# Kernel optimization log

Measured on AMD Instinct MI355X. Metric: run time of the kernel, lower is better.

## Reference

```python
import jax, jax.numpy as jnp
import numpy as np

DIM, HEADS, WH, WW = 96, 3, 7, 7
N = WH * WW            # 49 tokens per window
NW = 64                # windows per image (56x56 / 7x7)
B = 64                 # images
BNW = B * NW           # 4096


def _relative_position_index(Wh, Ww):
    coords = np.stack(np.meshgrid(np.arange(Wh), np.arange(Ww), indexing='ij'))
    coords = coords.reshape(2, -1)                       # (2, Wh*Ww)
    rel = coords[:, :, None] - coords[:, None, :]        # (2, N, N)
    rel = rel.transpose(1, 2, 0).copy()                  # (N, N, 2)
    rel[..., 0] += Wh - 1
    rel[..., 1] += Ww - 1
    rel[..., 0] *= 2 * Ww - 1
    return jnp.asarray(rel.sum(-1), dtype=jnp.int32)     # (N, N)


def setup_inputs() -> dict:
    key = jax.random.key(0)
    ks = jax.random.split(key, 8)
    x = jax.random.normal(ks[0], (BNW, N, DIM), dtype=jnp.float32)
    # shifted-window style additive mask: 0 where allowed, -100 where blocked
    mask = jnp.where(jax.random.uniform(ks[1], (NW, N, N)) < 0.9, 0.0, -100.0).astype(jnp.float32)
    qkv_w = jax.random.normal(ks[2], (3 * DIM, DIM), dtype=jnp.float32) * 0.02
    qkv_b = jnp.zeros((3 * DIM,), dtype=jnp.float32)
    proj_w = jax.random.normal(ks[3], (DIM, DIM), dtype=jnp.float32) * 0.02
    proj_b = jnp.zeros((DIM,), dtype=jnp.float32)
    rpb_table = jax.random.normal(ks[4], ((2 * WH - 1) * (2 * WW - 1), HEADS), dtype=jnp.float32) * 0.02
    rel_index = _relative_position_index(WH, WW)
    return {"x": x, "mask": mask, "qkv_w": qkv_w, "qkv_b": qkv_b,
            "proj_w": proj_w, "proj_b": proj_b, "rpb_table": rpb_table,
            "rel_index": rel_index}


def reference(x, mask, qkv_w, qkv_b, proj_w, proj_b, rpb_table, rel_index):
    BnW, n, C = x.shape
    H = rpb_table.shape[-1]
    hd = C // H
    scale = hd ** -0.5
    qkv = (x @ qkv_w.T + qkv_b).reshape(BnW, n, 3, H, hd)
    qkv = jnp.transpose(qkv, (2, 0, 3, 1, 4))            # (3, BnW, H, N, hd)
    q, k, v = qkv[0] * scale, qkv[1], qkv[2]
    attn = jnp.einsum('bhnd,bhmd->bhnm', q, k)           # (BnW, H, N, N)
    bias = rpb_table[rel_index.reshape(-1)].reshape(n, n, H)
    attn = attn + jnp.transpose(bias, (2, 0, 1))[None]
    nW = mask.shape[0]
    attn = attn.reshape(BnW // nW, nW, H, n, n) + mask[None, :, None]
    attn = attn.reshape(BnW, H, n, n)
    # 'neg' softmax: sign(x) * softmax(|x|)
    attn = jnp.sign(attn) * jax.nn.softmax(jnp.abs(attn), axis=-1)
    out = jnp.einsum('bhnm,bhmd->bnhd', attn, v).reshape(BnW, n, C)
    return out @ proj_w.T + proj_b
```

## Files before the change

kernel.cpp:

```cpp
#include <hip/hip_runtime.h>
#include <math.h>

#define DIM    96
#define HEADS  3
#define NTOK   49
#define NWIN   64
#define SCALE  0.17677669529663687f
#define MW     2

#define PROJWB_OFFB 55296
#define TAB_OFFB    73728
#define FUSED_TAB_ELEMS (NWIN * HEADS * NTOK * NTOK)
#define BIAS_TAB_ELEMS  (HEADS * NTOK * NTOK)
#define WS_MODE2_NEED (TAB_OFFB + FUSED_TAB_ELEMS * 4)
#define WS_MODE1_NEED (TAB_OFFB + BIAS_TAB_ELEMS * 4)

#define WSTRIDE 12288
#define K_OFF   0
#define VT_OFF  6144
#define LDS_SHORTS (MW * WSTRIDE)

typedef float  f32x4   __attribute__((ext_vector_type(4)));
typedef __bf16 bf16x8  __attribute__((ext_vector_type(8)));
typedef short  short8  __attribute__((ext_vector_type(8)));
typedef __bf16 bf16x4  __attribute__((ext_vector_type(4)));
typedef short  short4v __attribute__((ext_vector_type(4)));

union U8 { short8  s; bf16x8 b; };
union U4 { short4v s; bf16x4 b; };

__device__ __forceinline__ int swz(int s) { return s ^ ((s >> 3) & 56); }

__device__ __forceinline__ unsigned short f2bf(float f) {
    __bf16 h = (__bf16)f;
    union { __bf16 h; unsigned short u; } v; v.h = h; return v.u;
}

__device__ __forceinline__ void ldcvt_g(const float* __restrict__ p, U8& u) {
    float4 f0 = *(const float4*)p;
    float4 f1 = *(const float4*)(p + 4);
    u.b[0] = (__bf16)f0.x; u.b[1] = (__bf16)f0.y; u.b[2] = (__bf16)f0.z; u.b[3] = (__bf16)f0.w;
    u.b[4] = (__bf16)f1.x; u.b[5] = (__bf16)f1.y; u.b[6] = (__bf16)f1.z; u.b[7] = (__bf16)f1.w;
}

__global__ __launch_bounds__(256)
void prep(const float* __restrict__ rpb, const int* __restrict__ rel,
          const float* __restrict__ mask,
          const float* __restrict__ qkv_w, const float* __restrict__ proj_w,
          unsigned short* __restrict__ qkv_wb, unsigned short* __restrict__ proj_wb,
          float* __restrict__ tab, int mode)
{
    int t = blockIdx.x * 256 + threadIdx.x;
    if (mode >= 1) {
        if (t < 3 * DIM * DIM) qkv_wb[t] = f2bf(qkv_w[t]);
        if (t < DIM * DIM)     proj_wb[t] = f2bf(proj_w[t]);
    }
    if (mode == 2) {
        if (t < FUSED_TAB_ELEMS) {
            int win = t / (HEADS * NTOK * NTOK);
            int rem = t - win * (HEADS * NTOK * NTOK);
            int h   = rem / (NTOK * NTOK);
            int ij  = rem - h * (NTOK * NTOK);
            int k = ij / NTOK, q = ij - k * NTOK;
            tab[t] = rpb[rel[q * NTOK + k] * HEADS + h] + mask[win * (NTOK * NTOK) + q * NTOK + k];
        }
    } else if (t < BIAS_TAB_ELEMS) {
        int h = t / (NTOK * NTOK), ij = t - h * (NTOK * NTOK);
        int k = ij / NTOK, q = ij - k * NTOK;
        tab[t] = rpb[rel[q * NTOK + k] * HEADS + h];
    }
}

template<int MODE>
__device__ __forceinline__ void ldw(const unsigned short* __restrict__ wb,
                                    const float* __restrict__ wf, int idx, U8& u) {
    if constexpr (MODE >= 1) u.s = *(const short8*)(wb + idx);
    else                     ldcvt_g(wf + idx, u);
}
template<int MODE>
__device__ __forceinline__ void ldw4(const unsigned short* __restrict__ wb,
                                     const float* __restrict__ wf, int idx, U4& u) {
    if constexpr (MODE >= 1) u.s = *(const short4v*)(wb + idx);
    else {
        float4 f = *(const float4*)(wf + idx);
        u.b[0] = (__bf16)f.x; u.b[1] = (__bf16)f.y; u.b[2] = (__bf16)f.z; u.b[3] = (__bf16)f.w;
    }
}

template<int MODE>
__global__ __launch_bounds__(256, 3)
void winattn(const float* __restrict__ x,
             const float* __restrict__ mask,
             const float* __restrict__ qkv_w,
             const float* __restrict__ qkv_b,
             const float* __restrict__ proj_w,
             const float* __restrict__ proj_b,
             const unsigned short* __restrict__ qkv_wb,
             const unsigned short* __restrict__ proj_wb,
             const float* __restrict__ tab,
             float* __restrict__ out, int nwin_tot)
{
    __shared__ __align__(16) unsigned short sbuf[LDS_SHORTS];

    const int tid  = threadIdx.x;
    const int lane = tid & 63;
    const int wave = __builtin_amdgcn_readfirstlane(tid >> 6);
    const int l15  = lane & 15;
    const int quad = lane >> 4;
    const int tokg = 16 * wave + l15;
    const int qcl  = (tokg < NTOK) ? tokg : (NTOK - 1);

    int bw[MW];
    const float* fmh[MW][3];
    const float* mww[MW];
    #pragma unroll
    for (int w = 0; w < MW; ++w) {
        int b = blockIdx.x * MW + w;
        bw[w] = (b < nwin_tot) ? b : (nwin_tot - 1);
        const int win = bw[w] & (NWIN - 1);
        #pragma unroll
        for (int h = 0; h < 3; ++h)
            fmh[w][h] = (MODE == 2) ? (tab + (size_t)(win * HEADS + h) * (NTOK * NTOK))
                                    : (tab + h * (NTOK * NTOK));
        mww[w] = mask + (size_t)win * (NTOK * NTOK);
    }

    U8 af[MW][3];
    #pragma unroll
    for (int w = 0; w < MW; ++w) {
        const float* xw = x + (size_t)bw[w] * (NTOK * DIM);
        #pragma unroll
        for (int s = 0; s < 3; ++s) {
            if (tokg < NTOK) ldcvt_g(xw + tokg * DIM + 32 * s + quad * 8, af[w][s]);
            else {
                #pragma unroll
                for (int j = 0; j < 8; ++j) af[w][s].b[j] = (__bf16)0.0f;
            }
        }
    }

    U4 qB[MW][3][2];
    U8 wpf[2][3];
    f32x4 qbp[2];
    #pragma unroll
    for (int s = 0; s < 3; ++s) {
        ldw<MODE>(qkv_wb, qkv_w, (l15) * DIM + 32 * s + quad * 8, wpf[0][s]);
        ldw<MODE>(qkv_wb, qkv_w, (16 + l15) * DIM + 32 * s + quad * 8, wpf[1][s]);
    }
    qbp[0] = *(const f32x4*)(qkv_b + quad * 4);
    qbp[1] = *(const f32x4*)(qkv_b + 16 + quad * 4);

    #pragma unroll
    for (int t = 0; t < 18; ++t) {
        f32x4 acc[MW];
        #pragma unroll
        for (int w = 0; w < MW; ++w) {
            f32x4 z = {0.f, 0.f, 0.f, 0.f};
            #pragma unroll
            for (int s = 0; s < 3; ++s)
                z = __builtin_amdgcn_mfma_f32_16x16x32_bf16(wpf[t & 1][s].b, af[w][s].b, z, 0, 0, 0);
            acc[w] = z;
        }
        f32x4 qb = qbp[t & 1];
        if (t + 2 < 18) {
            #pragma unroll
            for (int s = 0; s < 3; ++s)
                ldw<MODE>(qkv_wb, qkv_w, (16 * (t + 2) + l15) * DIM + 32 * s + quad * 8, wpf[t & 1][s]);
            qbp[t & 1] = *(const f32x4*)(qkv_b + 16 * (t + 2) + quad * 4);
        }
        if (t < 6) {
            const int h = t >> 1, half = t & 1;
            #pragma unroll
            for (int w = 0; w < MW; ++w)
                #pragma unroll
                for (int r = 0; r < 4; ++r)
                    qB[w][h][half].b[r] = (__bf16)((acc[w][r] + qb[r]) * SCALE);
        } else if (t < 12) {
            const int tt = t - 6, h = tt >> 1, dc = tt & 1;
            #pragma unroll
            for (int w = 0; w < MW; ++w) {
                U4 pk;
                #pragma unroll
                for (int r = 0; r < 4; ++r) pk.b[r] = (__bf16)(acc[w][r] + qb[r]);
                *(short4v*)(sbuf + swz(w * WSTRIDE + K_OFF + h * 2048 + tokg * 32 + dc * 16 + quad * 4)) = pk.s;
            }
        } else {
            const int tt = t - 12, h = tt >> 1, dc = tt & 1;
            #pragma unroll
            for (int w = 0; w < MW; ++w)
                #pragma unroll
                for (int r = 0; r < 4; ++r)
                    sbuf[swz(w * WSTRIDE + VT_OFF + h * 2048 + (dc * 16 + quad * 4 + r) * 64 + tokg)] =
                        f2bf(acc[w][r] + qb[r]);
        }
    }

    float tv[2][4][4];
    #pragma unroll
    for (int t = 0; t < 4; ++t)
        #pragma unroll
        for (int r = 0; r < 4; ++r) {
            const int k = 16 * t + quad * 4 + r;
            float v = fmh[0][0][k * NTOK + qcl];
            if constexpr (MODE != 2) {
                const int kcl = (k < NTOK) ? k : (NTOK - 1);
                v += mww[0][qcl * NTOK + kcl];
            }
            tv[0][t][r] = v;
        }

    __syncthreads();

    U4 oB[MW][3][2];
    #pragma unroll
    for (int h = 0; h < 3; ++h) {
        #pragma unroll
        for (int w = 0; w < MW; ++w) {
            const int it = h * MW + w;
            const int base = w * WSTRIDE;
            f32x4 st[4];
            #pragma unroll
            for (int t = 0; t < 4; ++t) {
                U4 k0, k1;
                k0.s = *(const short4v*)(sbuf + swz(base + K_OFF + h * 2048 + (16 * t + l15) * 32 + quad * 4));
                k1.s = *(const short4v*)(sbuf + swz(base + K_OFF + h * 2048 + (16 * t + l15) * 32 + 16 + quad * 4));
                f32x4 z = {0.f, 0.f, 0.f, 0.f};
                z = __builtin_amdgcn_mfma_f32_16x16x16bf16_1k(k0.s, qB[w][h][0].s, z, 0, 0, 0);
                z = __builtin_amdgcn_mfma_f32_16x16x16bf16_1k(k1.s, qB[w][h][1].s, z, 0, 0, 0);
                st[t] = z;
            }
            if (it < 3 * MW - 1) {
                const int hn = (it + 1) / MW, wn = (it + 1) % MW;
                #pragma unroll
                for (int t = 0; t < 4; ++t)
                    #pragma unroll
                    for (int r = 0; r < 4; ++r) {
                        const int k = 16 * t + quad * 4 + r;
                        float v = fmh[wn][hn][k * NTOK + qcl];
                        if constexpr (MODE != 2) {
                            const int kcl = (k < NTOK) ? k : (NTOK - 1);
                            v += mww[wn][qcl * NTOK + kcl];
                        }
                        tv[(it + 1) & 1][t][r] = v;
                    }
            }
            float sval[4][4];
            float mx = -1e30f;
            #pragma unroll
            for (int t = 0; t < 4; ++t)
                #pragma unroll
                for (int r = 0; r < 4; ++r) {
                    const int k = 16 * t + quad * 4 + r;
                    float s_ = st[t][r] + tv[it & 1][t][r];
                    sval[t][r] = s_;
                    if (k < NTOK) mx = fmaxf(mx, fabsf(s_));
                }
            mx = fmaxf(mx, __shfl_xor(mx, 16));
            mx = fmaxf(mx, __shfl_xor(mx, 32));
            float sm = 0.f;
            U4 pa[4];
            #pragma unroll
            for (int t = 0; t < 4; ++t)
                #pragma unroll
                for (int r = 0; r < 4; ++r) {
                    const int k = 16 * t + quad * 4 + r;
                    const float s_ = sval[t][r];
                    const float e = (k < NTOK) ? __expf(fabsf(s_) - mx) : 0.f;
                    sm += e;
                    pa[t].b[r] = (__bf16)((s_ > 0.f) ? e : ((s_ < 0.f) ? -e : 0.f));
                }
            sm += __shfl_xor(sm, 16);
            sm += __shfl_xor(sm, 32);
            const float invl = 1.f / sm;
            #pragma unroll
            for (int dp = 0; dp < 2; ++dp) {
                f32x4 o = {0.f, 0.f, 0.f, 0.f};
                #pragma unroll
                for (int t = 0; t < 4; ++t) {
                    U4 vf;
                    vf.s = *(const short4v*)(sbuf + swz(base + VT_OFF + h * 2048 + (16 * dp + l15) * 64 + 16 * t + quad * 4));
                    o = __builtin_amdgcn_mfma_f32_16x16x16bf16_1k(vf.s, pa[t].s, o, 0, 0, 0);
                }
                #pragma unroll
                for (int r = 0; r < 4; ++r)
                    oB[w][h][dp].b[r] = (__bf16)(o[r] * invl);
            }
        }
    }

    {
        U4 w4pf[2][6];
        f32x4 pbp[2];
        #pragma unroll
        for (int kc = 0; kc < 6; ++kc)
            ldw4<MODE>(proj_wb, proj_w, l15 * DIM + 16 * kc + quad * 4, w4pf[0][kc]);
        pbp[0] = *(const f32x4*)(proj_b + quad * 4);

        #pragma unroll
        for (int tc = 0; tc < 6; ++tc) {
            if (tc + 1 < 6) {
                #pragma unroll
                for (int kc = 0; kc < 6; ++kc)
                    ldw4<MODE>(proj_wb, proj_w, (16 * (tc + 1) + l15) * DIM + 16 * kc + quad * 4,
                               w4pf[(tc + 1) & 1][kc]);
                pbp[(tc + 1) & 1] = *(const f32x4*)(proj_b + 16 * (tc + 1) + quad * 4);
            }
            f32x4 acc[MW];
            #pragma unroll
            for (int w = 0; w < MW; ++w) acc[w] = f32x4{0.f, 0.f, 0.f, 0.f};
            #pragma unroll
            for (int kc = 0; kc < 6; ++kc)
                #pragma unroll
                for (int w = 0; w < MW; ++w)
                    acc[w] = __builtin_amdgcn_mfma_f32_16x16x16bf16_1k(
                        w4pf[tc & 1][kc].s, oB[w][kc >> 1][kc & 1].s, acc[w], 0, 0, 0);
            const f32x4 pb = pbp[tc & 1];
            #pragma unroll
            for (int w = 0; w < MW; ++w) {
                if (tokg < NTOK)
                    *(f32x4*)(out + (size_t)bw[w] * (NTOK * DIM) + tokg * DIM + 16 * tc + quad * 4) =
                        acc[w] + pb;
            }
        }
    }
}

extern "C" void kernel_launch(void* const* d_in, const int* in_sizes, int n_in,
                              void* d_out, int out_size, void* d_ws, size_t ws_size,
                              hipStream_t stream) {
    const float* x      = (const float*)d_in[0];
    const float* mask   = (const float*)d_in[1];
    const float* qkv_w  = (const float*)d_in[2];
    const float* qkv_b  = (const float*)d_in[3];
    const float* proj_w = (const float*)d_in[4];
    const float* proj_b = (const float*)d_in[5];
    const float* rpb    = (const float*)d_in[6];
    const int*   rel    = (const int*)d_in[7];
    float* outp         = (float*)d_out;

    int mode;
    if      (ws_size >= (size_t)WS_MODE2_NEED) mode = 2;
    else if (ws_size >= (size_t)WS_MODE1_NEED) mode = 1;
    else                                        mode = 0;

    unsigned short* qkv_wb  = (unsigned short*)d_ws;
    unsigned short* proj_wb = (unsigned short*)((char*)d_ws + PROJWB_OFFB);
    float* tab = (mode >= 1) ? (float*)((char*)d_ws + TAB_OFFB) : (float*)d_ws;

    const int npre = (mode == 2) ? FUSED_TAB_ELEMS
                   : (mode == 1) ? 3 * DIM * DIM
                                 : BIAS_TAB_ELEMS;
    prep<<<(npre + 255) / 256, 256, 0, stream>>>(rpb, rel, mask, qkv_w, proj_w,
                                                 qkv_wb, proj_wb, tab, mode);

    const int n_windows = in_sizes[0] / (NTOK * DIM);
    const int nb = (n_windows + MW - 1) / MW;
    if (mode == 2)
        winattn<2><<<nb, 256, 0, stream>>>(x, mask, qkv_w, qkv_b, proj_w, proj_b,
                                           qkv_wb, proj_wb, tab, outp, n_windows);
    else if (mode == 1)
        winattn<1><<<nb, 256, 0, stream>>>(x, mask, qkv_w, qkv_b, proj_w, proj_b,
                                           qkv_wb, proj_wb, tab, outp, n_windows);
    else
        winattn<0><<<nb, 256, 0, stream>>>(x, mask, qkv_w, qkv_b, proj_w, proj_b,
                                           qkv_wb, proj_wb, tab, outp, n_windows);
}
```

Measured before the change: 211.7 us.

## Compute QKV per head into double-buffered LDS, interleaved with attention

Result: slower. 277.7 us (+31.2%).

```diff
diff --git a/kernel.cpp b/kernel.cpp
--- a/kernel.cpp
+++ b/kernel.cpp
@@ -15,10 +15,10 @@
 #define WS_MODE2_NEED (TAB_OFFB + FUSED_TAB_ELEMS * 4)
 #define WS_MODE1_NEED (TAB_OFFB + BIAS_TAB_ELEMS * 4)
 
-#define WSTRIDE 12288
-#define K_OFF   0
-#define VT_OFF  6144
-#define LDS_SHORTS (MW * WSTRIDE)
+#define BUFSTRIDE 8192
+#define WSTRIDE   4096
+#define VT_OFF    2048
+#define LDS_SHORTS (2 * BUFSTRIDE)
 
 typedef float  f32x4   __attribute__((ext_vector_type(4)));
 typedef __bf16 bf16x8  __attribute__((ext_vector_type(8)));
@@ -88,7 +88,7 @@
 }
 
 template<int MODE>
-__global__ __launch_bounds__(256, 3)
+__global__ __launch_bounds__(256, 4)
 void winattn(const float* __restrict__ x,
              const float* __restrict__ mask,
              const float* __restrict__ qkv_w,
@@ -139,61 +139,66 @@
         }
     }
 
-    U4 qB[MW][3][2];
-    U8 wpf[2][3];
-    f32x4 qbp[2];
-    #pragma unroll
-    for (int s = 0; s < 3; ++s) {
-        ldw<MODE>(qkv_wb, qkv_w, (l15) * DIM + 32 * s + quad * 8, wpf[0][s]);
-        ldw<MODE>(qkv_wb, qkv_w, (16 + l15) * DIM + 32 * s + quad * 8, wpf[1][s]);
-    }
-    qbp[0] = *(const f32x4*)(qkv_b + quad * 4);
-    qbp[1] = *(const f32x4*)(qkv_b + 16 + quad * 4);
-
-    #pragma unroll
-    for (int t = 0; t < 18; ++t) {
-        f32x4 acc[MW];
-        #pragma unroll
-        for (int w = 0; w < MW; ++w) {
-            f32x4 z = {0.f, 0.f, 0.f, 0.f};
-            #pragma unroll
-            for (int s = 0; s < 3; ++s)
-                z = __builtin_amdgcn_mfma_f32_16x16x32_bf16(wpf[t & 1][s].b, af[w][s].b, z, 0, 0, 0);
-            acc[w] = z;
-        }
-        f32x4 qb = qbp[t & 1];
-        if (t + 2 < 18) {
-            #pragma unroll
-            for (int s = 0; s < 3; ++s)
-                ldw<MODE>(qkv_wb, qkv_w, (16 * (t + 2) + l15) * DIM + 32 * s + quad * 8, wpf[t & 1][s]);
-            qbp[t & 1] = *(const f32x4*)(qkv_b + 16 * (t + 2) + quad * 4);
-        }
-        if (t < 6) {
-            const int h = t >> 1, half = t & 1;
-            #pragma unroll
-            for (int w = 0; w < MW; ++w)
-                #pragma unroll
-                for (int r = 0; r < 4; ++r)
-                    qB[w][h][half].b[r] = (__bf16)((acc[w][r] + qb[r]) * SCALE);
-        } else if (t < 12) {
-            const int tt = t - 6, h = tt >> 1, dc = tt & 1;
+    U4 qB[2][MW][2];
+
+    auto stage = [&](const int h, const int hb) {
+        const int tl[6] = {2*h, 2*h + 1, 6 + 2*h, 7 + 2*h, 12 + 2*h, 13 + 2*h};
+        const int bb = hb * BUFSTRIDE;
+        U8 wpf[2][3];
+        f32x4 qbp[2];
+        #pragma unroll
+        for (int s = 0; s < 3; ++s) {
+            ldw<MODE>(qkv_wb, qkv_w, (16 * tl[0] + l15) * DIM + 32 * s + quad * 8, wpf[0][s]);
+            ldw<MODE>(qkv_wb, qkv_w, (16 * tl[1] + l15) * DIM + 32 * s + quad * 8, wpf[1][s]);
+        }
+        qbp[0] = *(const f32x4*)(qkv_b + 16 * tl[0] + quad * 4);
+        qbp[1] = *(const f32x4*)(qkv_b + 16 * tl[1] + quad * 4);
+        #pragma unroll
+        for (int i = 0; i < 6; ++i) {
+            f32x4 acc[MW];
             #pragma unroll
             for (int w = 0; w < MW; ++w) {
-                U4 pk;
-                #pragma unroll
-                for (int r = 0; r < 4; ++r) pk.b[r] = (__bf16)(acc[w][r] + qb[r]);
-                *(short4v*)(sbuf + swz(w * WSTRIDE + K_OFF + h * 2048 + tokg * 32 + dc * 16 + quad * 4)) = pk.s;
-            }
-        } else {
-            const int tt = t - 12, h = tt >> 1, dc = tt & 1;
-            #pragma unroll
-            for (int w = 0; w < MW; ++w)
-                #pragma unroll
-                for (int r = 0; r < 4; ++r)
-                    sbuf[swz(w * WSTRIDE + VT_OFF + h * 2048 + (dc * 16 + quad * 4 + r) * 64 + tokg)] =
-                        f2bf(acc[w][r] + qb[r]);
-        }
-    }
+                f32x4 z = {0.f, 0.f, 0.f, 0.f};
+                #pragma unroll
+                for (int s = 0; s < 3; ++s)
+                    z = __builtin_amdgcn_mfma_f32_16x16x32_bf16(wpf[i & 1][s].b, af[w][s].b, z, 0, 0, 0);
+                acc[w] = z;
+            }
+            const f32x4 qb = qbp[i & 1];
+            if (i + 2 < 6) {
+                #pragma unroll
+                for (int s = 0; s < 3; ++s)
+                    ldw<MODE>(qkv_wb, qkv_w, (16 * tl[i + 2] + l15) * DIM + 32 * s + quad * 8, wpf[i & 1][s]);
+                qbp[i & 1] = *(const f32x4*)(qkv_b + 16 * tl[i + 2] + quad * 4);
+            }
+            if (i < 2) {
+                #pragma unroll
+                for (int w = 0; w < MW; ++w)
+                    #pragma unroll
+                    for (int r = 0; r < 4; ++r)
+                        qB[hb][w][i].b[r] = (__bf16)((acc[w][r] + qb[r]) * SCALE);
+            } else if (i < 4) {
+                const int dc = i - 2;
+                #pragma unroll
+                for (int w = 0; w < MW; ++w) {
+                    U4 pk;
+                    #pragma unroll
+                    for (int r = 0; r < 4; ++r) pk.b[r] = (__bf16)(acc[w][r] + qb[r]);
+                    *(short4v*)(sbuf + swz(bb + w * WSTRIDE + tokg * 32 + dc * 16 + quad * 4)) = pk.s;
+                }
+            } else {
+                const int dc = i - 4;
+                #pragma unroll
+                for (int w = 0; w < MW; ++w)
+                    #pragma unroll
+                    for (int r = 0; r < 4; ++r)
+                        sbuf[swz(bb + w * WSTRIDE + VT_OFF + (dc * 16 + quad * 4 + r) * 64 + tokg)] =
+                            f2bf(acc[w][r] + qb[r]);
+            }
+        }
+    };
+
+    stage(0, 0);
 
     float tv[2][4][4];
     #pragma unroll
@@ -214,21 +219,23 @@
     U4 oB[MW][3][2];
     #pragma unroll
     for (int h = 0; h < 3; ++h) {
+        const int rb = (h & 1) * BUFSTRIDE;
         #pragma unroll
         for (int w = 0; w < MW; ++w) {
             const int it = h * MW + w;
-            const int base = w * WSTRIDE;
+            const int base = rb + w * WSTRIDE;
             f32x4 st[4];
             #pragma unroll
             for (int t = 0; t < 4; ++t) {
                 U4 k0, k1;
-                k0.s = *(const short4v*)(sbuf + swz(base + K_OFF + h * 2048 + (16 * t + l15) * 32 + quad * 4));
-                k1.s = *(const short4v*)(sbuf + swz(base + K_OFF + h * 2048 + (16 * t + l15) * 32 + 16 + quad * 4));
+                k0.s = *(const short4v*)(sbuf + swz(base + (16 * t + l15) * 32 + quad * 4));
+                k1.s = *(const short4v*)(sbuf + swz(base + (16 * t + l15) * 32 + 16 + quad * 4));
                 f32x4 z = {0.f, 0.f, 0.f, 0.f};
-                z = __builtin_amdgcn_mfma_f32_16x16x16bf16_1k(k0.s, qB[w][h][0].s, z, 0, 0, 0);
-                z = __builtin_amdgcn_mfma_f32_16x16x16bf16_1k(k1.s, qB[w][h][1].s, z, 0, 0, 0);
+                z = __builtin_amdgcn_mfma_f32_16x16x16bf16_1k(k0.s, qB[h & 1][w][0].s, z, 0, 0, 0);
+                z = __builtin_amdgcn_mfma_f32_16x16x16bf16_1k(k1.s, qB[h & 1][w][1].s, z, 0, 0, 0);
                 st[t] = z;
             }
+            if (w == 0 && h < 2) stage(h + 1, (h + 1) & 1);
             if (it < 3 * MW - 1) {
                 const int hn = (it + 1) / MW, wn = (it + 1) % MW;
                 #pragma unroll
@@ -278,7 +285,7 @@
                 #pragma unroll
                 for (int t = 0; t < 4; ++t) {
                     U4 vf;
-                    vf.s = *(const short4v*)(sbuf + swz(base + VT_OFF + h * 2048 + (16 * dp + l15) * 64 + 16 * t + quad * 4));
+                    vf.s = *(const short4v*)(sbuf + swz(base + VT_OFF + (16 * dp + l15) * 64 + 16 * t + quad * 4));
                     o = __builtin_amdgcn_mfma_f32_16x16x16bf16_1k(vf.s, pa[t].s, o, 0, 0, 0);
                 }
                 #pragma unroll
@@ -286,6 +293,7 @@
                     oB[w][h][dp].b[r] = (__bf16)(o[r] * invl);
             }
         }
+        if (h < 2) __syncthreads();
     }
 
     {
```
